# Kernel optimization log

Hardware: AMD Instinct MI355X
Metric: run time of the kernel (lower is better)

Reference implementation:

```python
import jax, jax.numpy as jnp
import numpy as np

B, T, D = 4, 4096, 1024

def setup_inputs() -> dict:
    key = jax.random.key(0)
    ks = jax.random.split(key, 6)
    x = jax.random.normal(ks[0], (B, T, D), dtype=jnp.float32)
    mask = jax.random.randint(ks[1], (B, T), 0, 2).astype(bool)
    # torch nn.Linear init scale ~ 1/sqrt(fan_in); exact init unimportant for correctness baseline
    s = 1.0 / np.sqrt(D)
    W_qkv = jax.random.normal(ks[2], (3 * D, D), dtype=jnp.float32) * s
    b_qkv = jax.random.normal(ks[3], (3 * D,), dtype=jnp.float32) * s
    W_out = jax.random.normal(ks[4], (D, D), dtype=jnp.float32) * s
    b_out = jax.random.normal(ks[5], (D,), dtype=jnp.float32) * s
    return {"x": x, "mask": mask, "W_qkv": W_qkv, "b_qkv": b_qkv, "W_out": W_out, "b_out": b_out}

def reference(x, mask, W_qkv, b_qkv, W_out, b_out):
    # qkv projection: (B,T,D) @ (D,3D) + (3D,)
    qkv = jnp.einsum('btd,ed->bte', x, W_qkv) + b_qkv
    q, k, v = jnp.split(qkv, 3, axis=-1)  # each (B,T,D)
    q = q / jnp.linalg.norm(q, axis=-1, keepdims=True)
    k = k / jnp.linalg.norm(k, axis=-1, keepdims=True)
    k = jnp.where(mask[..., None], 0.0, k)  # masked_fill(mask, 0)
    kv = jnp.sum(k * v, axis=-2, keepdims=True)  # (B,1,D) global feature sum
    out = kv * q  # (B,T,D)
    return jnp.einsum('btd,ed->bte', out, W_out) + b_out
```

## Files before the change

### kernel.cpp

```cpp
#include <hip/hip_runtime.h>
#include <stdint.h>


typedef short  short8   __attribute__((ext_vector_type(8)));
typedef float  floatx16 __attribute__((ext_vector_type(16)));

#define BM 128
#define BN 128
#define BK 64

__device__ __forceinline__ void async16(const void* g, void* l) {
  __builtin_amdgcn_global_load_lds((const __attribute__((address_space(1))) void*)g,
                                   (__attribute__((address_space(3))) void*)l, 16, 0, 0);
}

__device__ __forceinline__ uint16_t f2bf(float f) {
  union { float f; uint32_t u; } x; x.f = f;
  uint32_t u = x.u;
  return (uint16_t)((u + 0x7fffu + ((u >> 16) & 1u)) >> 16);
}
__device__ __forceinline__ float bf2f(uint16_t h) {
  union { uint32_t u; float f; } x; x.u = ((uint32_t)h) << 16; return x.f;
}
__device__ __forceinline__ uint32_t pack2(float a, float b) {
  return (uint32_t)f2bf(a) | ((uint32_t)f2bf(b) << 16);
}
__device__ __forceinline__ void upk8(uint4 u, float* f) {
  f[0]=bf2f((uint16_t)u.x); f[1]=bf2f((uint16_t)(u.x>>16));
  f[2]=bf2f((uint16_t)u.y); f[3]=bf2f((uint16_t)(u.y>>16));
  f[4]=bf2f((uint16_t)u.z); f[5]=bf2f((uint16_t)(u.z>>16));
  f[6]=bf2f((uint16_t)u.w); f[7]=bf2f((uint16_t)(u.w>>16));
}

__global__ __launch_bounds__(256) void cvt3(
    const float* __restrict__ a, uint16_t* __restrict__ ao, int na,
    const float* __restrict__ b, uint16_t* __restrict__ bo, int nb,
    const float* __restrict__ c, uint16_t* __restrict__ co, int nc) {
  int i = blockIdx.x * 256 + threadIdx.x;
  const float* in; uint16_t* out; int j = i;
  if (j < na) { in = a; out = ao; }
  else {
    j -= na;
    if (j < nb) { in = b; out = bo; }
    else { j -= nb; if (j >= nc) return; in = c; out = co; }
  }
  const float4* p = (const float4*)in;
  float4 u = p[(size_t)j * 2], v = p[(size_t)j * 2 + 1];
  uint4 o;
  o.x = pack2(u.x, u.y); o.y = pack2(u.z, u.w);
  o.z = pack2(v.x, v.y); o.w = pack2(v.z, v.w);
  ((uint4*)out)[j] = o;
}

__global__ __launch_bounds__(256, 2) void gemm1(
    const uint16_t* __restrict__ A, const uint16_t* __restrict__ Bw,
    const float* __restrict__ bias, uint16_t* __restrict__ Cb,
    int N, int K)
{
  __shared__ __align__(16) uint16_t As[BM * BK];
  __shared__ __align__(16) uint16_t Bs[BN * BK];
  const int tid = threadIdx.x;
  const int wave = tid >> 6, lane = tid & 63;
  const int l31 = lane & 31, khalf = lane >> 5;
  const int wm = wave & 1, wn = wave >> 1;
  const int id = blockIdx.x;
  const int xcd = id & 7, w = id >> 3;
  const int tileM = (w / 3) * BM;
  const int tileN = (xcd * 3 + (w % 3)) * BN;

  const int srow = wave * 8 + (lane >> 3);
  const int skc  = (lane & 7) ^ (lane >> 3);
  const uint16_t* gA = A  + (size_t)(tileM + srow) * K + skc * 8;
  const uint16_t* gB = Bw + (size_t)(tileN + srow) * K + skc * 8;
  char* lA = (char*)As + wave * 64 * 16;
  char* lB = (char*)Bs + wave * 64 * 16;

  floatx16 acc[2][2];
#pragma unroll
  for (int mi = 0; mi < 2; mi++)
#pragma unroll
    for (int ni = 0; ni < 2; ni++)
#pragma unroll
      for (int r = 0; r < 16; r++) acc[mi][ni][r] = 0.f;

  const int arow0 = wm * 64 + l31;
  const int brow0 = wn * 64 + l31;

  for (int k0 = 0; k0 < K; k0 += BK) {
#pragma unroll
    for (int s = 0; s < 4; s++) {
      async16(gA + k0 + s * 32 * K, lA + s * 4096);
      async16(gB + k0 + s * 32 * K, lB + s * 4096);
    }
    __syncthreads();
#pragma unroll
    for (int ks = 0; ks < 4; ks++) {
      const int kc = khalf + ks * 2;
      short8 af[2], bfr[2];
#pragma unroll
      for (int mi = 0; mi < 2; mi++) {
        int r = arow0 + mi * 32;
        af[mi] = *(const short8*)&As[(r * 8 + (kc ^ (r & 7))) * 8];
      }
#pragma unroll
      for (int ni = 0; ni < 2; ni++) {
        int r = brow0 + ni * 32;
        bfr[ni] = *(const short8*)&Bs[(r * 8 + (kc ^ (r & 7))) * 8];
      }
#pragma unroll
      for (int mi = 0; mi < 2; mi++)
#pragma unroll
        for (int ni = 0; ni < 2; ni++)
          acc[mi][ni] = __builtin_amdgcn_mfma_f32_32x32x16_bf16(af[mi], bfr[ni], acc[mi][ni], 0, 0, 0);
    }
    __syncthreads();
  }

#pragma unroll
  for (int mi = 0; mi < 2; mi++) {
    int rbase = tileM + wm * 64 + mi * 32 + 4 * khalf;
#pragma unroll
    for (int ni = 0; ni < 2; ni++) {
      int col = tileN + wn * 64 + ni * 32 + l31;
      float bv = bias[col];
#pragma unroll
      for (int reg = 0; reg < 16; reg++) {
        int row = rbase + (reg & 3) + 8 * (reg >> 2);
        Cb[(size_t)row * N + col] = f2bf(acc[mi][ni][reg] + bv);
      }
    }
  }
}

__global__ __launch_bounds__(256, 2) void gemm2(
    const uint16_t* __restrict__ qkv, const float* __restrict__ invq,
    const float* __restrict__ kv, const uint16_t* __restrict__ Bw,
    const float* __restrict__ bias, float* __restrict__ Cf)
{
  __shared__ __align__(16) uint16_t As[BM * BK];
  __shared__ __align__(16) uint16_t Bs[BN * BK];
  __shared__ __align__(16) float kvs[1024];
  const int tid = threadIdx.x;
  const int wave = tid >> 6, lane = tid & 63;
  const int l31 = lane & 31, khalf = lane >> 5;
  const int wm = wave & 1, wn = wave >> 1;
  const int id = blockIdx.x;
  const int tileM = (id >> 3) * BM;
  const int tileN = (id & 7) * BN;

  const int srow = wave * 8 + (lane >> 3);
  const int skc  = (lane & 7) ^ (lane >> 3);
  const uint16_t* gB = Bw + (size_t)(tileN + srow) * 1024 + skc * 8;
  char* lB = (char*)Bs + wave * 64 * 16;

  {
    int i = tid * 4;
    *(float4*)&kvs[i] = *(const float4*)(kv + ((tileM >> 12) << 10) + i);
  }
  float sinv[4];
#pragma unroll
  for (int s = 0; s < 4; s++) sinv[s] = invq[tileM + s * 32 + srow];

  floatx16 acc[2][2];
#pragma unroll
  for (int mi = 0; mi < 2; mi++)
#pragma unroll
    for (int ni = 0; ni < 2; ni++)
#pragma unroll
      for (int r = 0; r < 16; r++) acc[mi][ni][r] = 0.f;

  const int arow0 = wm * 64 + l31;
  const int brow0 = wn * 64 + l31;
  const uint16_t* qbase = qkv + (size_t)(tileM + srow) * 3072 + skc * 8;

  __syncthreads();

  for (int k0 = 0; k0 < 1024; k0 += BK) {
#pragma unroll
    for (int s = 0; s < 4; s++)
      async16(gB + k0 + s * 32 * 1024, lB + s * 4096);
#pragma unroll
    for (int s = 0; s < 4; s++) {
      int d = k0 + skc * 8;
      uint4 qv = *(const uint4*)(qbase + (size_t)s * 32 * 3072 + k0);
      float4 k0v = *(const float4*)&kvs[d];
      float4 k1v = *(const float4*)&kvs[d + 4];
      float qf[8]; upk8(qv, qf);
      float sc = sinv[s];
      uint4 o;
      o.x = pack2(qf[0] * sc * k0v.x, qf[1] * sc * k0v.y);
      o.y = pack2(qf[2] * sc * k0v.z, qf[3] * sc * k0v.w);
      o.z = pack2(qf[4] * sc * k1v.x, qf[5] * sc * k1v.y);
      o.w = pack2(qf[6] * sc * k1v.z, qf[7] * sc * k1v.w);
      *(uint4*)((char*)As + (size_t)(s * 256 + wave * 64 + lane) * 16) = o;
    }
    __syncthreads();
#pragma unroll
    for (int ks = 0; ks < 4; ks++) {
      const int kc = khalf + ks * 2;
      short8 af[2], bfr[2];
#pragma unroll
      for (int mi = 0; mi < 2; mi++) {
        int r = arow0 + mi * 32;
        af[mi] = *(const short8*)&As[(r * 8 + (kc ^ (r & 7))) * 8];
      }
#pragma unroll
      for (int ni = 0; ni < 2; ni++) {
        int r = brow0 + ni * 32;
        bfr[ni] = *(const short8*)&Bs[(r * 8 + (kc ^ (r & 7))) * 8];
      }
#pragma unroll
      for (int mi = 0; mi < 2; mi++)
#pragma unroll
        for (int ni = 0; ni < 2; ni++)
          acc[mi][ni] = __builtin_amdgcn_mfma_f32_32x32x16_bf16(af[mi], bfr[ni], acc[mi][ni], 0, 0, 0);
    }
    __syncthreads();
  }

#pragma unroll
  for (int mi = 0; mi < 2; mi++) {
    int rbase = tileM + wm * 64 + mi * 32 + 4 * khalf;
#pragma unroll
    for (int ni = 0; ni < 2; ni++) {
      int col = tileN + wn * 64 + ni * 32 + l31;
      float bv = bias[col];
#pragma unroll
      for (int reg = 0; reg < 16; reg++) {
        int row = rbase + (reg & 3) + 8 * (reg >> 2);
        Cf[(size_t)row * 1024 + col] = acc[mi][ni][reg] + bv;
      }
    }
  }
}

__global__ __launch_bounds__(256) void detect_mask(const unsigned char* __restrict__ m,
                                                   int* __restrict__ flag) {
  int i = blockIdx.x * blockDim.x + threadIdx.x;
  int v = ((i & 3) != 0) ? (int)m[i] : 0;
  unsigned long long b = __ballot(v != 0);
  if ((threadIdx.x & 63) == 0 && b) atomicOr(flag, 1);
}

__global__ __launch_bounds__(256) void rownorm_kv(
    const uint16_t* __restrict__ qkv, const void* __restrict__ maskbuf,
    const int* __restrict__ flag, float* __restrict__ invq, float* __restrict__ kv)
{
  __shared__ float kvloc[1024];
  const int tid = threadIdx.x;
  for (int i = tid; i < 1024; i += 256) kvloc[i] = 0.f;
  __syncthreads();
  const int wave = tid >> 6, lane = tid & 63;
  const int b = blockIdx.x >> 7;
  const int chunk = blockIdx.x & 127;
  const int isU8 = *flag;
  const unsigned char* m8 = (const unsigned char*)maskbuf;
  const int* m32 = (const int*)maskbuf;

  float kvacc[16];
#pragma unroll
  for (int i = 0; i < 16; i++) kvacc[i] = 0.f;

  const int r0 = b * 4096 + chunk * 32 + wave * 8;
  for (int j = 0; j < 8; j++) {
    int r = r0 + j;
    const uint16_t* rp = qkv + (size_t)r * 3072;
    uint4 q0 = *(const uint4*)(rp + lane * 16);
    uint4 q1 = *(const uint4*)(rp + lane * 16 + 8);
    uint4 k0 = *(const uint4*)(rp + 1024 + lane * 16);
    uint4 k1 = *(const uint4*)(rp + 1024 + lane * 16 + 8);
    uint4 v0 = *(const uint4*)(rp + 2048 + lane * 16);
    uint4 v1 = *(const uint4*)(rp + 2048 + lane * 16 + 8);
    float qf[16], kf[16], vf[16];
    upk8(q0, qf); upk8(q1, qf + 8);
    upk8(k0, kf); upk8(k1, kf + 8);
    upk8(v0, vf); upk8(v1, vf + 8);
    float sq = 0.f, sk = 0.f;
#pragma unroll
    for (int i = 0; i < 16; i++) { sq = fmaf(qf[i], qf[i], sq); sk = fmaf(kf[i], kf[i], sk); }
    for (int off = 32; off; off >>= 1) { sq += __shfl_xor(sq, off); sk += __shfl_xor(sk, off); }
    float rq = rsqrtf(sq), rk = rsqrtf(sk);
    if (lane == 0) invq[r] = rq;
    int masked = isU8 ? (int)m8[r] : m32[r];
    if (!masked) {
#pragma unroll
      for (int i = 0; i < 16; i++) kvacc[i] = fmaf(kf[i] * rk, vf[i], kvacc[i]);
    }
  }
#pragma unroll
  for (int i = 0; i < 16; i++) atomicAdd(&kvloc[lane * 16 + i], kvacc[i]);
  __syncthreads();
  for (int i = tid; i < 1024; i += 256) atomicAdd(&kv[b * 1024 + i], kvloc[i]);
}

extern "C" void kernel_launch(void* const* d_in, const int* in_sizes, int n_in,
                              void* d_out, int out_size, void* d_ws, size_t ws_size,
                              hipStream_t stream) {
  const float* x     = (const float*)d_in[0];
  const void*  mask  = d_in[1];
  const float* W_qkv = (const float*)d_in[2];
  const float* b_qkv = (const float*)d_in[3];
  const float* W_out = (const float*)d_in[4];
  const float* b_out = (const float*)d_in[5];
  float* out = (float*)d_out;

  const int BT = 4 * 4096;
  const int D  = 1024;

  char* ws = (char*)d_ws;
  size_t off = 0;
  auto alloc = [&](size_t bytes) { size_t r = off; off += (bytes + 255) & ~(size_t)255; return r; };
  size_t o_xb   = alloc((size_t)BT * D * 2);
  size_t o_qkvb = alloc((size_t)BT * 3 * D * 2);
  size_t o_wq   = alloc((size_t)3 * D * D * 2);
  size_t o_wo   = alloc((size_t)D * D * 2);
  size_t o_kv   = alloc((size_t)4 * D * 4 + 256);
  size_t o_invq = alloc((size_t)BT * 4);

  uint16_t* xb   = (uint16_t*)(ws + o_xb);
  uint16_t* qkvb = (uint16_t*)(ws + o_qkvb);
  uint16_t* wq   = (uint16_t*)(ws + o_wq);
  uint16_t* wo   = (uint16_t*)(ws + o_wo);
  float*    kv   = (float*)(ws + o_kv);
  int*      flag = (int*)(ws + o_kv + (size_t)4 * D * 4);
  float*    invq = (float*)(ws + o_invq);

  hipMemsetAsync(ws + o_kv, 0, (size_t)4 * D * 4 + 256, stream);
  {
    int na = BT * D / 8, nb = 3 * D * D / 8, nc = D * D / 8;
    int tot = na + nb + nc;
    cvt3<<<dim3((tot + 255) / 256), 256, 0, stream>>>(x, xb, na, W_qkv, wq, nb, W_out, wo, nc);
  }
  detect_mask<<<dim3(64), 256, 0, stream>>>((const unsigned char*)mask, flag);
  gemm1<<<dim3(3072), 256, 0, stream>>>(xb, wq, b_qkv, qkvb, 3 * D, D);
  rownorm_kv<<<dim3(512), 256, 0, stream>>>(qkvb, mask, flag, invq, kv);
  gemm2<<<dim3(1024), 256, 0, stream>>>(qkvb, invq, kv, wo, b_out, out);
}
```

Measured before the change: 333.3 us.

## Fold kv scaling into per-batch output weights and apply q-norm in epilogue

Rather than scaling each q tile by invq and kv in registers inside gemm2's K loop, a new scale_w kernel builds a per-batch weight copy W_out*kv in bf16. gemm2 then streams raw q and the scaled weights into LDS with async global-to-LDS loads, and applies invq as a row scale in the epilogue. This removes the synchronous load, convert and pack work from the GEMM main loop and lets A loads go async. The cost is an extra 8 MB weight buffer, one more kernel launch, bf16 rounding of the scaled weights, and per-element invq reads in the epilogue. It also adds an unroll-2 hint in rownorm_kv.

```diff
diff --git a/kernel.cpp b/kernel.cpp
--- a/kernel.cpp
+++ b/kernel.cpp
@@ -134,12 +134,11 @@
 
 __global__ __launch_bounds__(256, 2) void gemm2(
     const uint16_t* __restrict__ qkv, const float* __restrict__ invq,
-    const float* __restrict__ kv, const uint16_t* __restrict__ Bw,
-    const float* __restrict__ bias, float* __restrict__ Cf)
+    const uint16_t* __restrict__ Wp, const float* __restrict__ bias,
+    float* __restrict__ Cf)
 {
   __shared__ __align__(16) uint16_t As[BM * BK];
   __shared__ __align__(16) uint16_t Bs[BN * BK];
-  __shared__ __align__(16) float kvs[1024];
   const int tid = threadIdx.x;
   const int wave = tid >> 6, lane = tid & 63;
   const int l31 = lane & 31, khalf = lane >> 5;
@@ -147,19 +146,15 @@
   const int id = blockIdx.x;
   const int tileM = (id >> 3) * BM;
   const int tileN = (id & 7) * BN;
+  const int batch = tileM >> 12;
 
   const int srow = wave * 8 + (lane >> 3);
   const int skc  = (lane & 7) ^ (lane >> 3);
-  const uint16_t* gB = Bw + (size_t)(tileN + srow) * 1024 + skc * 8;
+  const uint16_t* gA = qkv + (size_t)(tileM + srow) * 3072 + skc * 8;
+  const uint16_t* gB = Wp + (size_t)batch * 1024 * 1024
+                          + (size_t)(tileN + srow) * 1024 + skc * 8;
+  char* lA = (char*)As + wave * 64 * 16;
   char* lB = (char*)Bs + wave * 64 * 16;
-
-  {
-    int i = tid * 4;
-    *(float4*)&kvs[i] = *(const float4*)(kv + ((tileM >> 12) << 10) + i);
-  }
-  float sinv[4];
-#pragma unroll
-  for (int s = 0; s < 4; s++) sinv[s] = invq[tileM + s * 32 + srow];
 
   floatx16 acc[2][2];
 #pragma unroll
@@ -171,28 +166,12 @@
 
   const int arow0 = wm * 64 + l31;
   const int brow0 = wn * 64 + l31;
-  const uint16_t* qbase = qkv + (size_t)(tileM + srow) * 3072 + skc * 8;
-
-  __syncthreads();
 
   for (int k0 = 0; k0 < 1024; k0 += BK) {
 #pragma unroll
-    for (int s = 0; s < 4; s++)
-      async16(gB + k0 + s * 32 * 1024, lB + s * 4096);
-#pragma unroll
     for (int s = 0; s < 4; s++) {
-      int d = k0 + skc * 8;
-      uint4 qv = *(const uint4*)(qbase + (size_t)s * 32 * 3072 + k0);
-      float4 k0v = *(const float4*)&kvs[d];
-      float4 k1v = *(const float4*)&kvs[d + 4];
-      float qf[8]; upk8(qv, qf);
-      float sc = sinv[s];
-      uint4 o;
-      o.x = pack2(qf[0] * sc * k0v.x, qf[1] * sc * k0v.y);
-      o.y = pack2(qf[2] * sc * k0v.z, qf[3] * sc * k0v.w);
-      o.z = pack2(qf[4] * sc * k1v.x, qf[5] * sc * k1v.y);
-      o.w = pack2(qf[6] * sc * k1v.z, qf[7] * sc * k1v.w);
-      *(uint4*)((char*)As + (size_t)(s * 256 + wave * 64 + lane) * 16) = o;
+      async16(gA + k0 + (size_t)s * 32 * 3072, lA + s * 4096);
+      async16(gB + k0 + (size_t)s * 32 * 1024, lB + s * 4096);
     }
     __syncthreads();
 #pragma unroll
@@ -228,10 +207,30 @@
 #pragma unroll
       for (int reg = 0; reg < 16; reg++) {
         int row = rbase + (reg & 3) + 8 * (reg >> 2);
-        Cf[(size_t)row * 1024 + col] = acc[mi][ni][reg] + bv;
-      }
-    }
-  }
+        Cf[(size_t)row * 1024 + col] = fmaf(invq[row], acc[mi][ni][reg], bv);
+      }
+    }
+  }
+}
+
+__global__ __launch_bounds__(256) void scale_w(
+    const uint16_t* __restrict__ wo, const float* __restrict__ kv,
+    uint16_t* __restrict__ wp)
+{
+  int i = blockIdx.x * 256 + threadIdx.x;
+  int e = i << 3;
+  int b = e >> 20;
+  int k = e & 1023;
+  uint4 w = *(const uint4*)(wo + (e & 0xFFFFF));
+  float4 k0v = *(const float4*)(kv + (b << 10) + k);
+  float4 k1v = *(const float4*)(kv + (b << 10) + k + 4);
+  float wf[8]; upk8(w, wf);
+  uint4 o;
+  o.x = pack2(wf[0] * k0v.x, wf[1] * k0v.y);
+  o.y = pack2(wf[2] * k0v.z, wf[3] * k0v.w);
+  o.z = pack2(wf[4] * k1v.x, wf[5] * k1v.y);
+  o.w = pack2(wf[6] * k1v.z, wf[7] * k1v.w);
+  *(uint4*)(wp + e) = o;
 }
 
 __global__ __launch_bounds__(256) void detect_mask(const unsigned char* __restrict__ m,
@@ -262,6 +261,7 @@
   for (int i = 0; i < 16; i++) kvacc[i] = 0.f;
 
   const int r0 = b * 4096 + chunk * 32 + wave * 8;
+#pragma unroll 2
   for (int j = 0; j < 8; j++) {
     int r = r0 + j;
     const uint16_t* rp = qkv + (size_t)r * 3072;
@@ -314,6 +314,7 @@
   size_t o_qkvb = alloc((size_t)BT * 3 * D * 2);
   size_t o_wq   = alloc((size_t)3 * D * D * 2);
   size_t o_wo   = alloc((size_t)D * D * 2);
+  size_t o_wp   = alloc((size_t)4 * D * D * 2);
   size_t o_kv   = alloc((size_t)4 * D * 4 + 256);
   size_t o_invq = alloc((size_t)BT * 4);
 
@@ -321,6 +322,7 @@
   uint16_t* qkvb = (uint16_t*)(ws + o_qkvb);
   uint16_t* wq   = (uint16_t*)(ws + o_wq);
   uint16_t* wo   = (uint16_t*)(ws + o_wo);
+  uint16_t* wp   = (uint16_t*)(ws + o_wp);
   float*    kv   = (float*)(ws + o_kv);
   int*      flag = (int*)(ws + o_kv + (size_t)4 * D * 4);
   float*    invq = (float*)(ws + o_invq);
@@ -334,5 +336,6 @@
   detect_mask<<<dim3(64), 256, 0, stream>>>((const unsigned char*)mask, flag);
   gemm1<<<dim3(3072), 256, 0, stream>>>(xb, wq, b_qkv, qkvb, 3 * D, D);
   rownorm_kv<<<dim3(512), 256, 0, stream>>>(qkvb, mask, flag, invq, kv);
-  gemm2<<<dim3(1024), 256, 0, stream>>>(qkvb, invq, kv, wo, b_out, out);
-}
+  scale_w<<<dim3(4 * D * D / 8 / 256), 256, 0, stream>>>(wo, kv, wp);
+  gemm2<<<dim3(1024), 256, 0, stream>>>(qkvb, invq, wp, b_out, out);
+}
```

Result: no change. 332.4 us (-0.2%).
